# Performance work log

Hardware: AMD Instinct MI355X
Metric: run time of the kernel (lower is better)

The kernel has to match this reference:

```python
import jax, jax.numpy as jnp
import numpy as np
import math

B, S, D, H = 2, 2048, 2048, 16
HD = D // H  # head_dim = 128


def _rope_tables(seq_len, head_dim, theta=10000.0):
    inv = 1.0 / (theta ** (np.arange(0, head_dim, 2, dtype=np.float32) / head_dim))
    t = np.arange(seq_len, dtype=np.float32)
    freqs = np.outer(t, inv)  # [S, HD/2]
    return jnp.asarray(np.cos(freqs)), jnp.asarray(np.sin(freqs))


def setup_inputs() -> dict:
    key = jax.random.key(0)
    ks = jax.random.split(key, 6)
    std = 1.0 / math.sqrt(D)
    x = jax.random.normal(ks[0], (B, S, D), dtype=jnp.float32)
    wq_w = jax.random.normal(ks[1], (D, D), dtype=jnp.float32) * std
    wk_w = jax.random.normal(ks[2], (D, D), dtype=jnp.float32) * std
    wv_w = jax.random.normal(ks[3], (D, D), dtype=jnp.float32) * std
    wo_w = jax.random.normal(ks[4], (D, D), dtype=jnp.float32) * std
    zb = jnp.zeros((D,), dtype=jnp.float32)
    fc, fs = _rope_tables(S, HD)
    return {"x": x, "wq_w": wq_w, "wq_b": zb, "wk_w": wk_w, "wk_b": zb,
            "wv_w": wv_w, "wv_b": zb, "wo_w": wo_w, "wo_b": zb,
            "freqs_cos": fc, "freqs_sin": fs}


def _apply_rope(q, k, cos, sin):
    # q, k: [B, S, H, HD]; cos/sin: [S, HD/2] -> broadcast [1, S, 1, HD/2]
    cos = cos[None, :, None, :]
    sin = sin[None, :, None, :]

    def rot(t):
        tr, ti = t[..., 0::2], t[..., 1::2]
        orr = tr * cos - ti * sin
        oi = tr * sin + ti * cos
        return jnp.stack([orr, oi], axis=-1).reshape(t.shape)

    return rot(q), rot(k)


def reference(x, wq_w, wq_b, wk_w, wk_b, wv_w, wv_b, wo_w, wo_b, freqs_cos, freqs_sin):
    b, s, d = x.shape
    q = (x @ wq_w.T + wq_b).reshape(b, s, H, HD)
    k = (x @ wk_w.T + wk_b).reshape(b, s, H, HD)
    v = (x @ wv_w.T + wv_b).reshape(b, s, H, HD)
    q, k = _apply_rope(q, k, freqs_cos[:s], freqs_sin[:s])
    q = q.transpose(0, 2, 1, 3)  # [B,H,S,HD]
    k = k.transpose(0, 2, 1, 3)
    v = v.transpose(0, 2, 1, 3)
    scale = math.sqrt(HD)
    scores = jnp.einsum('bhqd,bhkd->bhqk', q, k) / scale
    causal = jnp.tril(jnp.ones((s, s), dtype=bool))
    scores = jnp.where(causal[None, None], scores, jnp.float32(-jnp.inf))
    attn = jax.nn.softmax(scores, axis=-1)
    out = jnp.einsum('bhqk,bhkd->bhqd', attn, v)
    out = out.transpose(0, 2, 1, 3).reshape(b, s, d)
    out = out @ wo_w.T + wo_b
    return out, k, v
```

## Files before the change

kernel.cpp:

```cpp
#include <hip/hip_runtime.h>

#define B_  2
#define S_  2048
#define D_  2048
#define H_  16
#define HD_ 128

#define QSCALE 0.1275174319003887f

typedef __attribute__((ext_vector_type(4))) float  f32x4;
typedef __attribute__((ext_vector_type(8))) short  short8;
typedef __attribute__((ext_vector_type(8))) __bf16 bf16x8;
typedef __attribute__((ext_vector_type(4))) float  floatv4;
typedef __attribute__((ext_vector_type(4))) unsigned short ushortv4;

__device__ inline unsigned short f2bf(float f) {
  unsigned int u = __builtin_bit_cast(unsigned int, f);
  u += 0x7fffu + ((u >> 16) & 1u);
  return (unsigned short)(u >> 16);
}

__device__ inline void gld16(void* lds, const void* g) {
  __builtin_amdgcn_global_load_lds(
      (const __attribute__((address_space(1))) unsigned int*)g,
      (__attribute__((address_space(3))) unsigned int*)lds, 16, 0, 0);
}

__device__ inline bf16x8 lds_frag_b(const void* p) {
  return __builtin_bit_cast(bf16x8, *(const short8*)p);
}

__global__ void cvt_all(const float* __restrict__ x,
                        const float* __restrict__ w0, const float* __restrict__ w1,
                        const float* __restrict__ w2, const float* __restrict__ w3,
                        unsigned short* __restrict__ xb,
                        unsigned short* __restrict__ wb0, unsigned short* __restrict__ wb1,
                        unsigned short* __restrict__ wb2, unsigned short* __restrict__ wb3) {
  int i = blockIdx.x * 256 + threadIdx.x;
  const float* s; unsigned short* d; int off;
  if (i < 2097152) { s = x; d = xb; off = i; }
  else {
    int j = i - 2097152;
    int r = j >> 20; off = j & 1048575;
    s = (r == 0) ? w0 : (r == 1) ? w1 : (r == 2) ? w2 : w3;
    d = (r == 0) ? wb0 : (r == 1) ? wb1 : (r == 2) ? wb2 : wb3;
  }
  floatv4 v = ((const floatv4*)s)[off];
  ushortv4 o;
  o.x = f2bf(v.x); o.y = f2bf(v.y); o.z = f2bf(v.z); o.w = f2bf(v.w);
  ((ushortv4*)d)[off] = o;
}

template<int MI0, int NJ0>
__device__ inline void quad_mm(f32x4 (&acc)[4][4], const bf16x8 (&af)[2][2], const bf16x8 (&bf)[2][2]) {
#pragma unroll
  for (int mi = 0; mi < 2; ++mi)
#pragma unroll
    for (int nj = 0; nj < 2; ++nj)
#pragma unroll
      for (int ks = 0; ks < 2; ++ks)
        acc[MI0 + mi][NJ0 + nj] =
            __builtin_amdgcn_mfma_f32_16x16x32_bf16(af[mi][ks], bf[nj][ks], acc[MI0 + mi][NJ0 + nj], 0, 0, 0);
}

__device__ inline void stage(char* ldsbuf, int chunk, const char* gtile, int w, long thrOff) {
  gld16(ldsbuf + chunk * 8192 + w * 1024, gtile + (long)chunk * 64 * 4096 + thrOff);
}

#define RDF(dst, buf, baserow)                                                          \
  do {                                                                                  \
    int _r0 = (baserow);                                                                \
    _Pragma("unroll") for (int _ii = 0; _ii < 2; ++_ii) {                               \
      int _row = _r0 + _ii * 16;                                                        \
      _Pragma("unroll") for (int _ks = 0; _ks < 2; ++_ks)                               \
          dst[_ii][_ks] = lds_frag_b((buf) + _row * 128 + ((_ks * 64 + quad * 16) ^ xsw)); \
    }                                                                                   \
  } while (0)

#define GBAR() __builtin_amdgcn_s_barrier()
#define LGK0()                                                 \
  do {                                                         \
    asm volatile("s_waitcnt lgkmcnt(0)" ::: "memory");         \
    __builtin_amdgcn_sched_barrier(0);                         \
  } while (0)

template<int MODE>
__global__ __launch_bounds__(512, 1)
void gemm8p(const unsigned short* __restrict__ A,
            const unsigned short* __restrict__ W,
            const float* __restrict__ b0, const float* __restrict__ b1, const float* __restrict__ b2,
            float* __restrict__ CQ,
            float* __restrict__ CK,
            float* __restrict__ v_out,
            int nbx) {
  __shared__ __attribute__((aligned(16))) char smem[98304];
  char* As0 = smem;
  char* As1 = smem + 32768;
  char* Bs0 = smem + 65536;
  char* Bs1 = smem + 81920;

  const int t = threadIdx.x, w = t >> 6, lane = t & 63;
  const int quad = lane >> 4, l16 = lane & 15;
  const int wm = (w >> 1) * 64, wn = (w & 1) * 64;
  const int xsw = (l16 & 7) << 4;

  const int nwg = gridDim.x, q8 = nwg >> 3;
  const int wg = ((int)blockIdx.x & 7) * q8 + ((int)blockIdx.x >> 3);
  const int by = wg / nbx, bx = wg % nbx;
  const int m0 = by * 256, n0 = bx * 128;

  const char* Agl = (const char*)A + (size_t)m0 * 4096;
  const char* Wgl = (const char*)W + (size_t)n0 * 4096;
  const int sr = t >> 3;
  const long thrOff = (long)sr * 4096 + (((t & 7) * 16) ^ ((sr & 7) << 4));

#pragma unroll
  for (int c = 0; c < 4; ++c) stage(As0, c, Agl, w, thrOff);
#pragma unroll
  for (int c = 0; c < 2; ++c) stage(Bs0, c, Wgl, w, thrOff);
#pragma unroll
  for (int c = 0; c < 4; ++c) stage(As1, c, Agl + 128, w, thrOff);
#pragma unroll
  for (int c = 0; c < 2; ++c) stage(Bs1, c, Wgl + 128, w, thrOff);
  asm volatile("s_waitcnt vmcnt(6)" ::: "memory");
  GBAR();

  f32x4 acc[4][4] = {};

  for (int it = 0; it < 16; ++it) {
    int s0 = 2 * it + 2; if (s0 >= 32) s0 -= 2;
    int s1 = 2 * it + 3; if (s1 >= 32) s1 -= 2;
    const char* As0g = Agl + (long)s0 * 128;
    const char* Bs0g = Wgl + (long)s0 * 128;
    const char* As1g = Agl + (long)s1 * 128;
    const char* Bs1g = Wgl + (long)s1 * 128;
    bf16x8 a01[2][2], a23[2][2], b01[2][2], b23[2][2];

    RDF(a01, As0, wm + l16);
    RDF(b01, Bs0, wn + l16);
    GBAR(); LGK0();
    __builtin_amdgcn_s_setprio(1); quad_mm<0, 0>(acc, a01, b01); __builtin_amdgcn_s_setprio(0);
    GBAR();
    RDF(a23, As0, wm + 32 + l16);
    GBAR(); LGK0();
    __builtin_amdgcn_s_setprio(1); quad_mm<2, 0>(acc, a23, b01); __builtin_amdgcn_s_setprio(0);
    GBAR();
    RDF(b23, Bs0, wn + 32 + l16);
    stage(As0, 0, As0g, w, thrOff); stage(As0, 1, As0g, w, thrOff);
    GBAR(); LGK0();
    __builtin_amdgcn_s_setprio(1); quad_mm<0, 2>(acc, a01, b23); __builtin_amdgcn_s_setprio(0);
    GBAR();
    stage(As0, 2, As0g, w, thrOff); stage(As0, 3, As0g, w, thrOff);
    GBAR(); LGK0();
    __builtin_amdgcn_s_setprio(1); quad_mm<2, 2>(acc, a23, b23); __builtin_amdgcn_s_setprio(0);
    asm volatile("s_waitcnt vmcnt(4)" ::: "memory");
    GBAR();
    RDF(a01, As1, wm + l16);
    RDF(b01, Bs1, wn + l16);
    stage(Bs0, 0, Bs0g, w, thrOff); stage(Bs0, 1, Bs0g, w, thrOff);
    GBAR(); LGK0();
    __builtin_amdgcn_s_setprio(1); quad_mm<0, 0>(acc, a01, b01); __builtin_amdgcn_s_setprio(0);
    GBAR();
    RDF(a23, As1, wm + 32 + l16);
    GBAR(); LGK0();
    __builtin_amdgcn_s_setprio(1); quad_mm<2, 0>(acc, a23, b01); __builtin_amdgcn_s_setprio(0);
    GBAR();
    RDF(b23, Bs1, wn + 32 + l16);
    stage(As1, 0, As1g, w, thrOff); stage(As1, 1, As1g, w, thrOff);
    GBAR(); LGK0();
    __builtin_amdgcn_s_setprio(1); quad_mm<0, 2>(acc, a01, b23); __builtin_amdgcn_s_setprio(0);
    GBAR();
    stage(As1, 2, As1g, w, thrOff); stage(As1, 3, As1g, w, thrOff);
    stage(Bs1, 0, Bs1g, w, thrOff); stage(Bs1, 1, Bs1g, w, thrOff);
    GBAR(); LGK0();
    __builtin_amdgcn_s_setprio(1); quad_mm<2, 2>(acc, a23, b23); __builtin_amdgcn_s_setprio(0);
    asm volatile("s_waitcnt vmcnt(6)" ::: "memory");
    GBAR();
  }

  asm volatile("s_waitcnt vmcnt(0)" ::: "memory");

  if constexpr (MODE == 1) {
#pragma unroll
    for (int nj = 0; nj < 4; ++nj) {
      int col = n0 + wn + nj * 16 + l16;
      int sel = col >> 11;
      int cc  = col & 2047;
      const float* bp = (sel == 0) ? b0 : (sel == 1) ? b1 : b2;
      float bv = bp[cc];
#pragma unroll
      for (int mi = 0; mi < 4; ++mi)
#pragma unroll
        for (int r = 0; r < 4; ++r) {
          int row = m0 + wm + mi * 16 + quad * 4 + r;
          float v = acc[mi][nj][r] + bv;
          if (sel == 0) {
            CQ[(size_t)row * 2048 + cc] = v;
          } else if (sel == 1) {
            CK[(size_t)row * 2048 + cc] = v;
          } else {
            int s = row & 2047, bb = row >> 11;
            int hh = cc >> 7, d = cc & 127;
            v_out[((size_t)(bb * H_ + hh) * S_ + s) * HD_ + d] = v;
          }
        }
    }
  } else {
#pragma unroll
    for (int nj = 0; nj < 4; ++nj) {
      int col = n0 + wn + nj * 16 + l16;
      float bv = b0[col];
#pragma unroll
      for (int mi = 0; mi < 4; ++mi)
#pragma unroll
        for (int r = 0; r < 4; ++r) {
          int row = m0 + wm + mi * 16 + quad * 4 + r;
          CQ[(size_t)row * 2048 + col] = acc[mi][nj][r] + bv;
        }
    }
  }
}

__global__ void rope_kernel(const float* __restrict__ Qbuf,
                            const float* __restrict__ Kbuf,
                            const float* __restrict__ fc,
                            const float* __restrict__ fs,
                            unsigned short* __restrict__ Qa,
                            unsigned short* __restrict__ Ka,
                            float* __restrict__ k_out) {
  int idx = blockIdx.x * 256 + threadIdx.x;
  int i = idx & 63;
  int h = (idx >> 6) & (H_ - 1);
  int s = (idx >> 10) & (S_ - 1);
  int b = idx >> 21;
  size_t src = ((size_t)(b * S_ + s)) * D_ + h * HD_ + 2 * i;
  float2 q = *(const float2*)(Qbuf + src);
  float2 k = *(const float2*)(Kbuf + src);
  float c = fc[s * 64 + i], sn = fs[s * 64 + i];
  float qor = q.x * c - q.y * sn, qoi = q.x * sn + q.y * c;
  float kor = k.x * c - k.y * sn, koi = k.x * sn + k.y * c;
  size_t dst = ((size_t)((b * H_ + h) * S_ + s)) * HD_ + 2 * i;
  *(unsigned int*)(Qa + dst) = (unsigned int)f2bf(qor * QSCALE) | ((unsigned int)f2bf(qoi * QSCALE) << 16);
  *(unsigned int*)(Ka + dst) = (unsigned int)f2bf(kor) | ((unsigned int)f2bf(koi) << 16);
  *(float2*)(k_out + dst) = make_float2(kor, koi);
}

__global__ void vtrans_kernel(const float* __restrict__ Vsrc,
                              unsigned short* __restrict__ Vt) {
  __shared__ float tile[64][33];
  int t = threadIdx.x;
  int s0 = blockIdx.x * 64, d0 = blockIdx.y * 32, bh = blockIdx.z;
#pragma unroll
  for (int rr = 0; rr < 8; ++rr) {
    int sl = rr * 8 + (t >> 5), dl = t & 31;
    tile[sl][dl] = Vsrc[((size_t)(bh * S_ + s0 + sl)) * HD_ + d0 + dl];
  }
  __syncthreads();
#pragma unroll
  for (int rr = 0; rr < 8; ++rr) {
    int dl = rr * 4 + (t >> 6), sl = t & 63;
    Vt[((size_t)(bh * HD_ + d0 + dl)) * S_ + s0 + sl] = f2bf(tile[sl][dl]);
  }
}

__global__ __launch_bounds__(256, 2)
void attn_kernel(const unsigned short* __restrict__ Qa,
                 const unsigned short* __restrict__ Ka,
                 const unsigned short* __restrict__ Vt,
                 unsigned short* __restrict__ Oa) {
  __shared__ __attribute__((aligned(16))) unsigned short Ks[2][64 * 128];
  __shared__ __attribute__((aligned(16))) unsigned short Vs[128 * 64];
  __shared__ __attribute__((aligned(16))) unsigned short Ps[4][16 * 64];
  const int t = threadIdx.x, w = t >> 6, lane = t & 63;
  const int quad = lane >> 4, l16 = lane & 15;
  const int bid = blockIdx.x;
  const int bh = (bid & 7) + 8 * (bid >> 7);
  const int p  = (bid >> 3) & 15;
  const int b = bh >> 4, h = bh & 15;
  const unsigned short* Qp = Qa + (size_t)bh * S_ * HD_;
  const unsigned short* Kp = Ka + (size_t)bh * S_ * HD_;
  const unsigned short* Vp = Vt + (size_t)bh * HD_ * S_;
  const float NEGINF = -__builtin_inff();

  for (int part = 0; part < 2; ++part) {
    const int qs = part ? (31 - p) : p;
    const int q0 = qs * 64;
    const int ntmax = qs;

    __syncthreads();

#pragma unroll
    for (int j = 0; j < 4; ++j) {
      int o = (t + 256 * j) * 16;
      int row = o >> 8, cb = (o & 255) ^ ((row & 7) << 4);
      gld16((char*)Ks[0] + w * 1024 + j * 4096, (const char*)(Kp + (size_t)row * HD_) + cb);
    }
    bf16x8 qf[4];
#pragma unroll
    for (int kk = 0; kk < 4; ++kk)
      qf[kk] = *(const bf16x8*)(Qp + (size_t)(q0 + w * 16 + l16) * HD_ + kk * 32 + quad * 8);

    float m_i[4], l_i[4];
#pragma unroll
    for (int r = 0; r < 4; ++r) { m_i[r] = NEGINF; l_i[r] = 0.f; }
    f32x4 oacc[8] = {};
    int c = 0;

    for (int nt = 0; nt <= ntmax; ++nt) {
      __syncthreads();

#pragma unroll
      for (int j = 0; j < 4; ++j) {
        int o = (t + 256 * j) * 16;
        int vrow = o >> 7, vcb = (o & 127) ^ ((vrow & 7) << 4);
        gld16((char*)Vs + w * 1024 + j * 4096,
              (const char*)(Vp + (size_t)vrow * S_ + nt * 64) + vcb);
      }

      f32x4 sacc[4] = {};
      const char* Kc = (const char*)Ks[c];
#pragma unroll
      for (int j = 0; j < 4; ++j) {
        int krow = j * 16 + l16;
        const char* kbase = Kc + krow * 256;
        int ksw = (krow & 7) << 4;
#pragma unroll
        for (int kk = 0; kk < 4; ++kk) {
          bf16x8 kf = lds_frag_b(kbase + ((kk * 64 + quad * 16) ^ ksw));
          sacc[j] = __builtin_amdgcn_mfma_f32_16x16x32_bf16(qf[kk], kf, sacc[j], 0, 0, 0);
        }
      }

      const bool dotail = (nt == ntmax);
      float rowmax[4], rowsum[4];
#pragma unroll
      for (int r = 0; r < 4; ++r) rowmax[r] = NEGINF;
#pragma unroll
      for (int j = 0; j < 4; ++j) {
        int scol = nt * 64 + j * 16 + l16;
#pragma unroll
        for (int r = 0; r < 4; ++r) {
          float v = sacc[j][r];
          if (dotail && scol > q0 + w * 16 + quad * 4 + r) v = NEGINF;
          sacc[j][r] = v;
          rowmax[r] = fmaxf(rowmax[r], v);
        }
      }
#pragma unroll
      for (int off = 1; off < 16; off <<= 1)
#pragma unroll
        for (int r = 0; r < 4; ++r)
          rowmax[r] = fmaxf(rowmax[r], __shfl_xor(rowmax[r], off));

      bool grow = false;
#pragma unroll
      for (int r = 0; r < 4; ++r) grow = grow || (rowmax[r] > m_i[r]);
      if (__any(grow)) {
        float alpha[4];
#pragma unroll
        for (int r = 0; r < 4; ++r) {
          float mnew = fmaxf(m_i[r], rowmax[r]);
          alpha[r] = __builtin_amdgcn_exp2f(m_i[r] - mnew);
          m_i[r] = mnew;
          l_i[r] *= alpha[r];
        }
#pragma unroll
        for (int f = 0; f < 8; ++f)
#pragma unroll
          for (int r = 0; r < 4; ++r) oacc[f][r] *= alpha[r];
      }
#pragma unroll
      for (int r = 0; r < 4; ++r) rowsum[r] = 0.f;
#pragma unroll
      for (int j = 0; j < 4; ++j)
#pragma unroll
        for (int r = 0; r < 4; ++r) {
          float e = __builtin_amdgcn_exp2f(sacc[j][r] - m_i[r]);
          sacc[j][r] = e;
          rowsum[r] += e;
        }
#pragma unroll
      for (int off = 1; off < 16; off <<= 1)
#pragma unroll
        for (int r = 0; r < 4; ++r)
          rowsum[r] += __shfl_xor(rowsum[r], off);
#pragma unroll
      for (int r = 0; r < 4; ++r) l_i[r] += rowsum[r];

      __syncthreads();

      if (nt < ntmax) {
#pragma unroll
        for (int j = 0; j < 4; ++j) {
          int o = (t + 256 * j) * 16;
          int row = o >> 8, cb = (o & 255) ^ ((row & 7) << 4);
          gld16((char*)Ks[c ^ 1] + w * 1024 + j * 4096,
                (const char*)(Kp + (size_t)((nt + 1) * 64 + row) * HD_) + cb);
        }
      }

      char* Pw = (char*)&Ps[w][0];
#pragma unroll
      for (int j = 0; j < 4; ++j)
#pragma unroll
        for (int r = 0; r < 4; ++r) {
          int prow = quad * 4 + r;
          *(unsigned short*)(Pw + prow * 128 + ((2 * (j * 16 + l16)) ^ ((prow & 7) << 4))) = f2bf(sacc[j][r]);
        }
      asm volatile("s_waitcnt lgkmcnt(0)" ::: "memory");

      const char* Vb = (const char*)Vs;
      int psw = (l16 & 7) << 4;
#pragma unroll
      for (int s2 = 0; s2 < 2; ++s2) {
        bf16x8 pf = lds_frag_b(Pw + l16 * 128 + ((s2 * 64 + quad * 16) ^ psw));
#pragma unroll
        for (int f = 0; f < 8; ++f) {
          int vrow = f * 16 + l16;
          bf16x8 vf = lds_frag_b(Vb + vrow * 128 + ((s2 * 64 + quad * 16) ^ ((vrow & 7) << 4)));
          oacc[f] = __builtin_amdgcn_mfma_f32_16x16x32_bf16(pf, vf, oacc[f], 0, 0, 0);
        }
      }
      c ^= 1;
    }

    float invl[4];
#pragma unroll
    for (int r = 0; r < 4; ++r) invl[r] = 1.f / l_i[r];
#pragma unroll
    for (int f = 0; f < 8; ++f)
#pragma unroll
      for (int r = 0; r < 4; ++r) {
        int srow = q0 + w * 16 + quad * 4 + r;
        int d = f * 16 + l16;
        Oa[((size_t)(b * S_ + srow)) * D_ + h * HD_ + d] = f2bf(oacc[f][r] * invl[r]);
      }
  }
}

extern "C" void kernel_launch(void* const* d_in, const int* in_sizes, int n_in,
                              void* d_out, int out_size, void* d_ws, size_t ws_size,
                              hipStream_t stream) {
  const float* x    = (const float*)d_in[0];
  const float* wq_w = (const float*)d_in[1];
  const float* wq_b = (const float*)d_in[2];
  const float* wk_w = (const float*)d_in[3];
  const float* wk_b = (const float*)d_in[4];
  const float* wv_w = (const float*)d_in[5];
  const float* wv_b = (const float*)d_in[6];
  const float* wo_w = (const float*)d_in[7];
  const float* wo_b = (const float*)d_in[8];
  const float* fc   = (const float*)d_in[9];
  const float* fs   = (const float*)d_in[10];

  float* out = (float*)d_out;
  const size_t BSD = (size_t)B_ * S_ * D_;
  float* k_out = out + BSD;
  float* v_out = out + 2 * BSD;

  char* ws = (char*)d_ws;
  unsigned short* xb   = (unsigned short*)(ws);
  unsigned short* wqb  = (unsigned short*)(ws + 16777216);
  unsigned short* wkb  = (unsigned short*)(ws + 25165824);
  unsigned short* wvb  = (unsigned short*)(ws + 33554432);
  unsigned short* wob  = (unsigned short*)(ws + 41943040);
  float*          Kbuf = (float*)(ws + 50331648);
  unsigned short* Qat  = (unsigned short*)(ws + 83886080);
  unsigned short* Kat  = (unsigned short*)(ws + 100663296);
  unsigned short* Vt   = (unsigned short*)(ws + 117440512);
  unsigned short* Ab   = (unsigned short*)(ws + 134217728);

  float* Qbuf = out;

  cvt_all<<<24576, 256, 0, stream>>>(x, wq_w, wk_w, wv_w, wo_w, xb, wqb, wkb, wvb, wob);

  gemm8p<1><<<dim3(768), 512, 0, stream>>>(xb, wqb, wq_b, wk_b, wv_b,
                                           Qbuf, Kbuf, v_out, 48);

  rope_kernel<<<16384, 256, 0, stream>>>(Qbuf, Kbuf, fc, fs, Qat, Kat, k_out);
  vtrans_kernel<<<dim3(32, 4, 32), 256, 0, stream>>>(v_out, Vt);
  attn_kernel<<<512, 256, 0, stream>>>(Qat, Kat, Vt, Ab);

  gemm8p<0><<<dim3(256), 512, 0, stream>>>(Ab, wob, wo_b, nullptr, nullptr,
                                           out, nullptr, nullptr, 16);
}
```

Baseline: 462.3 us.

## Merge rope and V-transpose launches, add MFMA priority, make rescale unconditional

Combines the RoPE kernel and the V transpose kernel into one launch, with block ranges split by index, which removes one kernel launch and its tail. In the attention loop, wave priority is raised around both MFMA sections via s_setprio, and the online-softmax rescale is made branchless: alpha is always computed and applied to l and oacc, with no wave-wide vote. This trades the skip of the rescale when the max doesn't grow for straight-line code without the __any divergence check.

```diff
diff --git a/kernel.cpp b/kernel.cpp
--- a/kernel.cpp
+++ b/kernel.cpp
@@ -221,45 +221,48 @@
   }
 }
 
-__global__ void rope_kernel(const float* __restrict__ Qbuf,
+__global__ void rope_vtrans(const float* __restrict__ Qbuf,
                             const float* __restrict__ Kbuf,
                             const float* __restrict__ fc,
                             const float* __restrict__ fs,
                             unsigned short* __restrict__ Qa,
                             unsigned short* __restrict__ Ka,
-                            float* __restrict__ k_out) {
-  int idx = blockIdx.x * 256 + threadIdx.x;
-  int i = idx & 63;
-  int h = (idx >> 6) & (H_ - 1);
-  int s = (idx >> 10) & (S_ - 1);
-  int b = idx >> 21;
-  size_t src = ((size_t)(b * S_ + s)) * D_ + h * HD_ + 2 * i;
-  float2 q = *(const float2*)(Qbuf + src);
-  float2 k = *(const float2*)(Kbuf + src);
-  float c = fc[s * 64 + i], sn = fs[s * 64 + i];
-  float qor = q.x * c - q.y * sn, qoi = q.x * sn + q.y * c;
-  float kor = k.x * c - k.y * sn, koi = k.x * sn + k.y * c;
-  size_t dst = ((size_t)((b * H_ + h) * S_ + s)) * HD_ + 2 * i;
-  *(unsigned int*)(Qa + dst) = (unsigned int)f2bf(qor * QSCALE) | ((unsigned int)f2bf(qoi * QSCALE) << 16);
-  *(unsigned int*)(Ka + dst) = (unsigned int)f2bf(kor) | ((unsigned int)f2bf(koi) << 16);
-  *(float2*)(k_out + dst) = make_float2(kor, koi);
-}
-
-__global__ void vtrans_kernel(const float* __restrict__ Vsrc,
-                              unsigned short* __restrict__ Vt) {
+                            float* __restrict__ k_out,
+                            const float* __restrict__ Vsrc,
+                            unsigned short* __restrict__ Vt) {
   __shared__ float tile[64][33];
+  int bx = blockIdx.x;
   int t = threadIdx.x;
-  int s0 = blockIdx.x * 64, d0 = blockIdx.y * 32, bh = blockIdx.z;
-#pragma unroll
-  for (int rr = 0; rr < 8; ++rr) {
-    int sl = rr * 8 + (t >> 5), dl = t & 31;
-    tile[sl][dl] = Vsrc[((size_t)(bh * S_ + s0 + sl)) * HD_ + d0 + dl];
-  }
-  __syncthreads();
-#pragma unroll
-  for (int rr = 0; rr < 8; ++rr) {
-    int dl = rr * 4 + (t >> 6), sl = t & 63;
-    Vt[((size_t)(bh * HD_ + d0 + dl)) * S_ + s0 + sl] = f2bf(tile[sl][dl]);
+  if (bx < 16384) {
+    int idx = bx * 256 + t;
+    int i = idx & 63;
+    int h = (idx >> 6) & (H_ - 1);
+    int s = (idx >> 10) & (S_ - 1);
+    int b = idx >> 21;
+    size_t src = ((size_t)(b * S_ + s)) * D_ + h * HD_ + 2 * i;
+    float2 q = *(const float2*)(Qbuf + src);
+    float2 k = *(const float2*)(Kbuf + src);
+    float c = fc[s * 64 + i], sn = fs[s * 64 + i];
+    float qor = q.x * c - q.y * sn, qoi = q.x * sn + q.y * c;
+    float kor = k.x * c - k.y * sn, koi = k.x * sn + k.y * c;
+    size_t dst = ((size_t)((b * H_ + h) * S_ + s)) * HD_ + 2 * i;
+    *(unsigned int*)(Qa + dst) = (unsigned int)f2bf(qor * QSCALE) | ((unsigned int)f2bf(qoi * QSCALE) << 16);
+    *(unsigned int*)(Ka + dst) = (unsigned int)f2bf(kor) | ((unsigned int)f2bf(koi) << 16);
+    *(float2*)(k_out + dst) = make_float2(kor, koi);
+  } else {
+    int v = bx - 16384;
+    int s0 = (v & 31) * 64, d0 = ((v >> 5) & 3) * 32, bh = v >> 7;
+#pragma unroll
+    for (int rr = 0; rr < 8; ++rr) {
+      int sl = rr * 8 + (t >> 5), dl = t & 31;
+      tile[sl][dl] = Vsrc[((size_t)(bh * S_ + s0 + sl)) * HD_ + d0 + dl];
+    }
+    __syncthreads();
+#pragma unroll
+    for (int rr = 0; rr < 8; ++rr) {
+      int dl = rr * 4 + (t >> 6), sl = t & 63;
+      Vt[((size_t)(bh * HD_ + d0 + dl)) * S_ + s0 + sl] = f2bf(tile[sl][dl]);
+    }
   }
 }
 
@@ -319,6 +322,7 @@
 
       f32x4 sacc[4] = {};
       const char* Kc = (const char*)Ks[c];
+      __builtin_amdgcn_s_setprio(1);
 #pragma unroll
       for (int j = 0; j < 4; ++j) {
         int krow = j * 16 + l16;
@@ -330,9 +334,10 @@
           sacc[j] = __builtin_amdgcn_mfma_f32_16x16x32_bf16(qf[kk], kf, sacc[j], 0, 0, 0);
         }
       }
+      __builtin_amdgcn_s_setprio(0);
 
       const bool dotail = (nt == ntmax);
-      float rowmax[4], rowsum[4];
+      float rowmax[4], alpha[4], rowsum[4];
 #pragma unroll
       for (int r = 0; r < 4; ++r) rowmax[r] = NEGINF;
 #pragma unroll
@@ -351,26 +356,13 @@
 #pragma unroll
         for (int r = 0; r < 4; ++r)
           rowmax[r] = fmaxf(rowmax[r], __shfl_xor(rowmax[r], off));
-
-      bool grow = false;
-#pragma unroll
-      for (int r = 0; r < 4; ++r) grow = grow || (rowmax[r] > m_i[r]);
-      if (__any(grow)) {
-        float alpha[4];
-#pragma unroll
-        for (int r = 0; r < 4; ++r) {
-          float mnew = fmaxf(m_i[r], rowmax[r]);
-          alpha[r] = __builtin_amdgcn_exp2f(m_i[r] - mnew);
-          m_i[r] = mnew;
-          l_i[r] *= alpha[r];
-        }
-#pragma unroll
-        for (int f = 0; f < 8; ++f)
-#pragma unroll
-          for (int r = 0; r < 4; ++r) oacc[f][r] *= alpha[r];
-      }
-#pragma unroll
-      for (int r = 0; r < 4; ++r) rowsum[r] = 0.f;
+#pragma unroll
+      for (int r = 0; r < 4; ++r) {
+        float mnew = fmaxf(m_i[r], rowmax[r]);
+        alpha[r] = __builtin_amdgcn_exp2f(m_i[r] - mnew);
+        m_i[r] = mnew;
+        rowsum[r] = 0.f;
+      }
 #pragma unroll
       for (int j = 0; j < 4; ++j)
 #pragma unroll
@@ -385,7 +377,11 @@
         for (int r = 0; r < 4; ++r)
           rowsum[r] += __shfl_xor(rowsum[r], off);
 #pragma unroll
-      for (int r = 0; r < 4; ++r) l_i[r] += rowsum[r];
+      for (int r = 0; r < 4; ++r) l_i[r] = l_i[r] * alpha[r] + rowsum[r];
+#pragma unroll
+      for (int f = 0; f < 8; ++f)
+#pragma unroll
+        for (int r = 0; r < 4; ++r) oacc[f][r] *= alpha[r];
 
       __syncthreads();
 
@@ -411,6 +407,7 @@
 
       const char* Vb = (const char*)Vs;
       int psw = (l16 & 7) << 4;
+      __builtin_amdgcn_s_setprio(1);
 #pragma unroll
       for (int s2 = 0; s2 < 2; ++s2) {
         bf16x8 pf = lds_frag_b(Pw + l16 * 128 + ((s2 * 64 + quad * 16) ^ psw));
@@ -421,6 +418,7 @@
           oacc[f] = __builtin_amdgcn_mfma_f32_16x16x32_bf16(pf, vf, oacc[f], 0, 0, 0);
         }
       }
+      __builtin_amdgcn_s_setprio(0);
       c ^= 1;
     }
 
@@ -477,8 +475,8 @@
   gemm8p<1><<<dim3(768), 512, 0, stream>>>(xb, wqb, wq_b, wk_b, wv_b,
                                            Qbuf, Kbuf, v_out, 48);
 
-  rope_kernel<<<16384, 256, 0, stream>>>(Qbuf, Kbuf, fc, fs, Qat, Kat, k_out);
-  vtrans_kernel<<<dim3(32, 4, 32), 256, 0, stream>>>(v_out, Vt);
+  rope_vtrans<<<20480, 256, 0, stream>>>(Qbuf, Kbuf, fc, fs, Qat, Kat, k_out, v_out, Vt);
+
   attn_kernel<<<512, 256, 0, stream>>>(Qat, Kat, Vt, Ab);
 
   gemm8p<0><<<dim3(256), 512, 0, stream>>>(Ab, wob, wo_b, nullptr, nullptr,
```

After: 455.8 us. Within noise of the previous version (-1.4%).
